# Performance work log

Hardware: AMD Instinct MI355X
Metric: run time of the kernel (lower is better)

The kernel has to match this reference:

```python
import jax, jax.numpy as jnp
import numpy as np
import math

N, D, H, N_BINS, MAX_GRID = 4096, 512, 4, 32, 40

def setup_inputs() -> dict:
    key = jax.random.key(0)
    ks = jax.random.split(key, 12)
    vision_h = jax.random.normal(ks[0], (N, D), dtype=jnp.float32)
    patch_rows = jax.random.randint(ks[1], (N,), 0, MAX_GRID, dtype=jnp.int32)
    patch_cols = jax.random.randint(ks[2], (N,), 0, MAX_GRID, dtype=jnp.int32)
    pos_w = 0.01 * jax.random.normal(ks[3], (D, D), dtype=jnp.float32)
    q_w = 0.02 * jax.random.normal(ks[4], (D, D), dtype=jnp.float32)
    k_w = 0.02 * jax.random.normal(ks[5], (D, D), dtype=jnp.float32)
    v_w = 0.02 * jax.random.normal(ks[6], (D, D), dtype=jnp.float32)
    out_w = 0.02 * jax.random.normal(ks[7], (D, D), dtype=jnp.float32)
    dist_bias = 0.02 * jax.random.normal(ks[8], (H, N_BINS), dtype=jnp.float32)
    gamma_param = jnp.array(0.5, dtype=jnp.float32)
    ln_w = jnp.ones((D,), dtype=jnp.float32)
    ln_b = jnp.zeros((D,), dtype=jnp.float32)
    return {"vision_h": vision_h, "patch_rows": patch_rows, "patch_cols": patch_cols,
            "pos_w": pos_w, "q_w": q_w, "k_w": k_w, "v_w": v_w, "out_w": out_w,
            "dist_bias": dist_bias, "gamma_param": gamma_param, "ln_w": ln_w, "ln_b": ln_b}

def _sin_pe_1d(pos_f, half_dim):
    # pos_f: (N,) float. returns (N, half_dim) with even idx = sin, odd idx = cos
    freq = jnp.exp(jnp.arange(0, half_dim, 2, dtype=jnp.float32) * (-(math.log(10000.0) / half_dim)))
    ang = pos_f[:, None] * freq  # (N, half_dim//2)
    return jnp.stack([jnp.sin(ang), jnp.cos(ang)], axis=-1).reshape(pos_f.shape[0], half_dim)

def reference(vision_h, patch_rows, patch_cols, pos_w, q_w, k_w, v_w, out_w,
              dist_bias, gamma_param, ln_w, ln_b):
    n, d = vision_h.shape
    h = dist_bias.shape[0]
    hd = d // h
    n_bins = dist_bias.shape[1]
    half = d // 2

    rows_f = patch_rows.astype(jnp.float32)
    cols_f = patch_cols.astype(jnp.float32)
    pe = jnp.concatenate([_sin_pe_1d(rows_f, half), _sin_pe_1d(cols_f, half)], axis=-1)  # (N, D)

    h_pos = vision_h + pe @ pos_w.T
    Q = (h_pos @ q_w.T).reshape(n, h, hd).transpose(1, 0, 2)   # (H, N, hd)
    K = (h_pos @ k_w.T).reshape(n, h, hd).transpose(1, 0, 2)
    V = (vision_h @ v_w.T).reshape(n, h, hd).transpose(1, 0, 2)

    logits = jnp.einsum("hnd,hmd->hnm", Q, K) / math.sqrt(hd)   # (H, N, N)

    row_diff = rows_f[:, None] - rows_f[None, :]
    col_diff = cols_f[:, None] - cols_f[None, :]
    dist = jnp.sqrt(row_diff ** 2 + col_diff ** 2)              # (N, N)
    max_log_dist = math.log1p(MAX_GRID * math.sqrt(2.0))
    bins = (jnp.log1p(dist) / max_log_dist * (n_bins - 1)).astype(jnp.int32)
    bins = jnp.clip(bins, 0, n_bins - 1)
    rel_bias = dist_bias[:, bins]                               # (H, N, N)

    attn = jax.nn.softmax(logits + rel_bias, axis=-1)
    attn_out = jnp.einsum("hnm,hmd->hnd", attn, V).transpose(1, 0, 2).reshape(n, d)

    o = attn_out @ out_w.T
    mu = jnp.mean(o, axis=-1, keepdims=True)
    var = jnp.mean((o - mu) ** 2, axis=-1, keepdims=True)
    o_ln = (o - mu) / jnp.sqrt(var + 1e-5) * ln_w + ln_b

    gamma = jax.nn.softplus(gamma_param)
    return vision_h + gamma * o_ln
```

## Files before the change

kernel.cpp:

```cpp
#include <hip/hip_runtime.h>
#include <math.h>

#define N_TOK 4096
#define DMODEL 512
#define NHEAD 4
#define HDIM 128
#define NBINS 32
#define BQ 128
#define BK 64
#define NSPLIT 4
#define KV_PER_SPLIT (N_TOK / NSPLIT)
#define QKSTR 1024

typedef __attribute__((ext_vector_type(8))) short bf16x8;
typedef __attribute__((ext_vector_type(4))) float f32x4;
typedef __attribute__((ext_vector_type(8))) unsigned short u16x8;
typedef __attribute__((ext_vector_type(4))) unsigned short u16x4;

__device__ __forceinline__ unsigned short f2bf(float x) {
    unsigned int u = __float_as_uint(x);
    u += 0x7FFFu + ((u >> 16) & 1u);
    return (unsigned short)(u >> 16);
}
__device__ __forceinline__ float bf2f(unsigned short u) {
    return __uint_as_float(((unsigned int)u) << 16);
}

__global__ __launch_bounds__(256) void pe_prep(const int* __restrict__ rows,
                                               const int* __restrict__ cols,
                                               const float* __restrict__ vh,
                                               unsigned short* __restrict__ pe_bf,
                                               unsigned short* __restrict__ vh_bf) {
    int n = blockIdx.x, t = threadIdx.x;
    float pos = (float)((t < 128) ? rows[n] : cols[n]);
    int k = t & 127;
    float freq = expf(-0.035977892078032f * (float)(2 * k));
    float ang = pos * freq;
    int base = n * DMODEL + ((t < 128) ? 0 : 256) + 2 * k;
    pe_bf[base]     = f2bf(sinf(ang));
    pe_bf[base + 1] = f2bf(cosf(ang));
    float2 v = *(const float2*)&vh[(size_t)n * DMODEL + t * 2];
    vh_bf[(size_t)n * DMODEL + t * 2]     = f2bf(v.x);
    vh_bf[(size_t)n * DMODEL + t * 2 + 1] = f2bf(v.y);
}

__global__ __launch_bounds__(256) void wconv5(const float* __restrict__ w0, const float* __restrict__ w1,
                                              const float* __restrict__ w2, const float* __restrict__ w3,
                                              const float* __restrict__ w4,
                                              unsigned short* __restrict__ dstbase) {
    const float* srcs[5] = {w0, w1, w2, w3, w4};
    const float* src = srcs[blockIdx.y];
    unsigned short* dst = dstbase + (size_t)blockIdx.y * DMODEL * DMODEL;
    int idx = (blockIdx.x * 256 + threadIdx.x) * 4;
    float4 v = *(const float4*)&src[idx];
    u16x4 r;
    r[0] = f2bf(v.x); r[1] = f2bf(v.y); r[2] = f2bf(v.z); r[3] = f2bf(v.w);
    *(u16x4*)&dst[idx] = r;
}

template <bool ADD, bool BF16OUT>
__global__ __launch_bounds__(256) void gemm_mfma(const unsigned short* __restrict__ A,
                                                 const unsigned short* __restrict__ B,
                                                 const float* __restrict__ addv,
                                                 void* __restrict__ Cv,
                                                 int M, int N, int K,
                                                 float scaleA, float scaleB) {
    const int n0 = blockIdx.x * 64;
    const int j0 = blockIdx.y * 128;
    __shared__ unsigned short As[64][72];
    __shared__ unsigned short Bs[128][72];
    const int t    = threadIdx.x;
    const int wid  = t >> 6;
    const int wr   = wid >> 1, wc = wid & 1;
    const int lane = t & 63;
    const int lg   = lane >> 4, li = lane & 15;
    const int str  = t >> 3;
    const int sc   = (t & 7) * 8;

    f32x4 acc[2][4];
#pragma unroll
    for (int i = 0; i < 2; ++i)
#pragma unroll
        for (int j = 0; j < 4; ++j) acc[i][j] = (f32x4){0.f, 0.f, 0.f, 0.f};

    u16x8 areg[2], breg[4];
#pragma unroll
    for (int i = 0; i < 2; ++i)
        areg[i] = *(const u16x8*)&A[(size_t)(n0 + str + i * 32) * K + sc];
#pragma unroll
    for (int i = 0; i < 4; ++i)
        breg[i] = *(const u16x8*)&B[(size_t)(j0 + str + i * 32) * K + sc];

    for (int k0 = 0; k0 < K; k0 += 64) {
        __syncthreads();
#pragma unroll
        for (int i = 0; i < 2; ++i) *(u16x8*)&As[str + i * 32][sc] = areg[i];
#pragma unroll
        for (int i = 0; i < 4; ++i) *(u16x8*)&Bs[str + i * 32][sc] = breg[i];
        __syncthreads();
        if (k0 + 64 < K) {
#pragma unroll
            for (int i = 0; i < 2; ++i)
                areg[i] = *(const u16x8*)&A[(size_t)(n0 + str + i * 32) * K + k0 + 64 + sc];
#pragma unroll
            for (int i = 0; i < 4; ++i)
                breg[i] = *(const u16x8*)&B[(size_t)(j0 + str + i * 32) * K + k0 + 64 + sc];
        }
        __builtin_amdgcn_s_setprio(1);
#pragma unroll
        for (int kc = 0; kc < 2; ++kc) {
            bf16x8 af[2], bfr[4];
#pragma unroll
            for (int mf = 0; mf < 2; ++mf)
                af[mf] = *(const bf16x8*)&As[wr * 32 + mf * 16 + li][kc * 32 + lg * 8];
#pragma unroll
            for (int nf = 0; nf < 4; ++nf)
                bfr[nf] = *(const bf16x8*)&Bs[wc * 64 + nf * 16 + li][kc * 32 + lg * 8];
#pragma unroll
            for (int mf = 0; mf < 2; ++mf)
#pragma unroll
                for (int nf = 0; nf < 4; ++nf)
                    acc[mf][nf] = __builtin_amdgcn_mfma_f32_16x16x32_bf16(af[mf], bfr[nf], acc[mf][nf], 0, 0, 0);
        }
        __builtin_amdgcn_s_setprio(0);
    }
    const float scl = (j0 < 512) ? scaleA : scaleB;
#pragma unroll
    for (int mf = 0; mf < 2; ++mf) {
#pragma unroll
        for (int r = 0; r < 4; ++r) {
            const int row = n0 + wr * 32 + mf * 16 + lg * 4 + r;
#pragma unroll
            for (int nf = 0; nf < 4; ++nf) {
                const int col = j0 + wc * 64 + nf * 16 + li;
                float v = acc[mf][nf][r] * scl;
                if (ADD) v += addv[(size_t)row * N + col];
                if (BF16OUT) ((unsigned short*)Cv)[(size_t)row * N + col] = f2bf(v);
                else         ((float*)Cv)[(size_t)row * N + col] = v;
            }
        }
    }
}

__global__ __launch_bounds__(512, 2) void attn_mfma(const unsigned short* __restrict__ Qb,
                                                    const unsigned short* __restrict__ Kb,
                                                    const unsigned short* __restrict__ Vtb,
                                                    const int* __restrict__ prows,
                                                    const int* __restrict__ pcols,
                                                    const float* __restrict__ dist_bias,
                                                    unsigned short* __restrict__ Opart,
                                                    float* __restrict__ Mp,
                                                    float* __restrict__ Lp) {
    const int h  = blockIdx.y;
    const int n0 = blockIdx.x * BQ;
    const int sp = blockIdx.z;
    __shared__ unsigned short Ks[BK * HDIM];
    __shared__ unsigned short Vts[HDIM * BK];
    __shared__ unsigned short Ps[BQ][68];
    __shared__ unsigned short biasTb[3043];
    __shared__ int krs[BK], kcs[BK];

    const int t    = threadIdx.x;
    const int lane = t & 63;
    const int lg   = lane >> 4;
    const int li   = lane & 15;
    const int qbase = (t >> 6) * 16;

    for (int idx = t; idx < 3043; idx += 512) {
        float d  = sqrtf((float)idx);
        int bin  = (int)(log1pf(d) * (31.0f / 4.0529789877f));
        bin = bin > 31 ? 31 : bin;
        biasTb[idx] = f2bf(dist_bias[h * NBINS + bin]);
    }

    bf16x8 qf[4];
    {
        const unsigned short* qptr = &Qb[(size_t)(n0 + qbase + li) * QKSTR + h * HDIM];
#pragma unroll
        for (int kc = 0; kc < 4; ++kc)
            qf[kc] = *(const bf16x8*)&qptr[kc * 32 + lg * 8];
    }
    const int qrL = prows[n0 + qbase + li];
    const int qcL = pcols[n0 + qbase + li];

    float m_ = -1e30f;
    float l_ = 0.f;
    f32x4 accO[8];
#pragma unroll
    for (int dt = 0; dt < 8; ++dt) accO[dt] = (f32x4){0.f, 0.f, 0.f, 0.f};

    u16x8 kreg[2], vreg[2];
    int krreg = 0, kcreg = 0;
    const int ktr = t >> 4, kch = (t & 15) * 8;
    const int vtr = t >> 3, vch = (t & 7) * 8;

    const int kwofs0 = (ktr * 128 + kch) * 2;
    const int vwofs0 = (vtr * 64 + vch) * 2;

    int m0 = sp * KV_PER_SPLIT;
    {
#pragma unroll
        for (int i = 0; i < 2; ++i)
            kreg[i] = *(const u16x8*)&Kb[(size_t)(m0 + ktr + i * 32) * QKSTR + h * HDIM + kch];
#pragma unroll
        for (int i = 0; i < 2; ++i)
            vreg[i] = *(const u16x8*)&Vtb[(size_t)(h * HDIM + vtr + i * 64) * N_TOK + m0 + vch];
        if (t < BK) { krreg = prows[m0 + t]; kcreg = pcols[m0 + t]; }
    }

    for (int kb = 0; kb < KV_PER_SPLIT / BK; ++kb, m0 += BK) {
        __syncthreads();
#pragma unroll
        for (int i = 0; i < 2; ++i) {
            int ofs = (kwofs0 + i * 32 * 256) ^ ((ktr & 7) << 4);
            *(u16x8*)((char*)Ks + ofs) = kreg[i];
        }
#pragma unroll
        for (int i = 0; i < 2; ++i) {
            int ofs = (vwofs0 + i * 64 * 128) ^ ((vtr & 7) << 4);
            *(u16x8*)((char*)Vts + ofs) = vreg[i];
        }
        if (t < BK) { krs[t] = krreg; kcs[t] = kcreg; }
        __syncthreads();

        if (kb + 1 < KV_PER_SPLIT / BK) {
            const int m1 = m0 + BK;
#pragma unroll
            for (int i = 0; i < 2; ++i)
                kreg[i] = *(const u16x8*)&Kb[(size_t)(m1 + ktr + i * 32) * QKSTR + h * HDIM + kch];
#pragma unroll
            for (int i = 0; i < 2; ++i)
                vreg[i] = *(const u16x8*)&Vtb[(size_t)(h * HDIM + vtr + i * 64) * N_TOK + m1 + vch];
            if (t < BK) { krreg = prows[m1 + t]; kcreg = pcols[m1 + t]; }
        }

        f32x4 s[4];
        __builtin_amdgcn_s_setprio(1);
#pragma unroll
        for (int jt = 0; jt < 4; ++jt) {
            f32x4 acc = {0.f, 0.f, 0.f, 0.f};
#pragma unroll
            for (int kc = 0; kc < 4; ++kc) {
                int ofs = (((jt * 16 + li) * 128 + kc * 32 + lg * 8) * 2) ^ ((li & 7) << 4);
                bf16x8 kf = *(const bf16x8*)((const char*)Ks + ofs);
                acc = __builtin_amdgcn_mfma_f32_16x16x32_bf16(kf, qf[kc], acc, 0, 0, 0);
            }
            s[jt] = acc;
        }
        __builtin_amdgcn_s_setprio(0);

        float p[4][4];
#pragma unroll
        for (int jt = 0; jt < 4; ++jt) {
#pragma unroll
            for (int r = 0; r < 4; ++r) {
                int k  = jt * 16 + lg * 4 + r;
                int dr = qrL - krs[k], dc = qcL - kcs[k];
                p[jt][r] = s[jt][r] + bf2f(biasTb[dr * dr + dc * dc]);
            }
        }

        float t0 = fmaxf(fmaxf(p[0][0], p[0][1]), fmaxf(p[0][2], p[0][3]));
        float t1 = fmaxf(fmaxf(p[1][0], p[1][1]), fmaxf(p[1][2], p[1][3]));
        float t2 = fmaxf(fmaxf(p[2][0], p[2][1]), fmaxf(p[2][2], p[2][3]));
        float t3 = fmaxf(fmaxf(p[3][0], p[3][1]), fmaxf(p[3][2], p[3][3]));
        float pmax = fmaxf(fmaxf(t0, t1), fmaxf(t2, t3));
        pmax = fmaxf(pmax, __shfl_xor(pmax, 16));
        pmax = fmaxf(pmax, __shfl_xor(pmax, 32));

        if (!__all(pmax <= m_ + 8.0f)) {
            float mnew  = fmaxf(m_, pmax);
            float alpha = __expf(m_ - mnew);
            m_ = mnew;
            l_ *= alpha;
            float aq[4];
#pragma unroll
            for (int r = 0; r < 4; ++r)
                aq[r] = __shfl(alpha, (lane & 48) | (lg * 4 + r));
#pragma unroll
            for (int dt = 0; dt < 8; ++dt)
#pragma unroll
                for (int r = 0; r < 4; ++r) accO[dt][r] *= aq[r];
        }

        float rs = 0.f;
#pragma unroll
        for (int jt = 0; jt < 4; ++jt)
#pragma unroll
            for (int r = 0; r < 4; ++r) { p[jt][r] = __expf(p[jt][r] - m_); rs += p[jt][r]; }
        rs += __shfl_xor(rs, 16);
        rs += __shfl_xor(rs, 32);
        l_ += rs;

#pragma unroll
        for (int jt = 0; jt < 4; ++jt) {
            u16x4 w;
#pragma unroll
            for (int r = 0; r < 4; ++r) w[r] = f2bf(p[jt][r]);
            *(u16x4*)&Ps[qbase + li][jt * 16 + lg * 4] = w;
        }

        bf16x8 pf0 = *(const bf16x8*)&Ps[qbase + li][lg * 8];
        bf16x8 pf1 = *(const bf16x8*)&Ps[qbase + li][32 + lg * 8];
        __builtin_amdgcn_s_setprio(1);
#pragma unroll
        for (int dt = 0; dt < 8; ++dt) {
            int ofs0 = (((dt * 16 + li) * 64 + lg * 8) * 2) ^ ((li & 7) << 4);
            bf16x8 vf0 = *(const bf16x8*)((const char*)Vts + ofs0);
            bf16x8 vf1 = *(const bf16x8*)((const char*)Vts + (ofs0 ^ 64));
            accO[dt] = __builtin_amdgcn_mfma_f32_16x16x32_bf16(pf0, vf0, accO[dt], 0, 0, 0);
            accO[dt] = __builtin_amdgcn_mfma_f32_16x16x32_bf16(pf1, vf1, accO[dt], 0, 0, 0);
        }
        __builtin_amdgcn_s_setprio(0);
    }

    float linv[4];
#pragma unroll
    for (int r = 0; r < 4; ++r)
        linv[r] = __shfl(l_, (lane & 48) | (lg * 4 + r));
#pragma unroll
    for (int r = 0; r < 4; ++r) {
        float inv = 1.0f / linv[r];
        int row = n0 + qbase + lg * 4 + r;
#pragma unroll
        for (int dt = 0; dt < 8; ++dt)
            Opart[(size_t)sp * N_TOK * DMODEL + (size_t)row * DMODEL + h * HDIM + dt * 16 + li] =
                f2bf(accO[dt][r] * inv);
    }
    if (lane < 16) {
        int row = n0 + qbase + lane;
        Mp[((size_t)sp * NHEAD + h) * N_TOK + row] = m_;
        Lp[((size_t)sp * NHEAD + h) * N_TOK + row] = l_;
    }
}

__global__ __launch_bounds__(256) void combine_kernel(const unsigned short* __restrict__ Opart,
                                                      const float* __restrict__ Mp,
                                                      const float* __restrict__ Lp,
                                                      unsigned short* __restrict__ outbf) {
    int n = blockIdx.x, t = threadIdx.x;
#pragma unroll
    for (int d0 = t; d0 < DMODEL; d0 += 256) {
        int h = d0 >> 7;
        float mm[NSPLIT], ll[NSPLIT];
        float m = -1e30f;
#pragma unroll
        for (int s = 0; s < NSPLIT; ++s) {
            mm[s] = Mp[((size_t)s * NHEAD + h) * N_TOK + n];
            ll[s] = Lp[((size_t)s * NHEAD + h) * N_TOK + n];
            m = fmaxf(m, mm[s]);
        }
        float acc = 0.f, lsum = 0.f;
#pragma unroll
        for (int s = 0; s < NSPLIT; ++s) {
            float a = __expf(mm[s] - m) * ll[s];
            lsum += a;
            acc += a * bf2f(Opart[(size_t)s * N_TOK * DMODEL + (size_t)n * DMODEL + d0]);
        }
        outbf[(size_t)n * DMODEL + d0] = f2bf(acc / lsum);
    }
}

__global__ __launch_bounds__(256) void final_kernel(const float* __restrict__ o,
                                                    const float* __restrict__ vh,
                                                    const float* __restrict__ lnw,
                                                    const float* __restrict__ lnb,
                                                    const float* __restrict__ gparam,
                                                    float* __restrict__ out) {
    int n = blockIdx.x, t = threadIdx.x;
    size_t base = (size_t)n * DMODEL;
    float x0 = o[base + t], x1 = o[base + t + 256];
    __shared__ float red[4];
    float v = x0 + x1;
#pragma unroll
    for (int off = 32; off > 0; off >>= 1) v += __shfl_down(v, off, 64);
    if ((t & 63) == 0) red[t >> 6] = v;
    __syncthreads();
    float mu = (red[0] + red[1] + red[2] + red[3]) * (1.0f / 512.0f);
    __syncthreads();
    float d0 = x0 - mu, d1 = x1 - mu;
    v = d0 * d0 + d1 * d1;
#pragma unroll
    for (int off = 32; off > 0; off >>= 1) v += __shfl_down(v, off, 64);
    if ((t & 63) == 0) red[t >> 6] = v;
    __syncthreads();
    float var  = (red[0] + red[1] + red[2] + red[3]) * (1.0f / 512.0f);
    float rstd = rsqrtf(var + 1e-5f);
    float gamma = log1pf(expf(gparam[0]));
    out[base + t]       = vh[base + t]       + gamma * (d0 * rstd * lnw[t]       + lnb[t]);
    out[base + t + 256] = vh[base + t + 256] + gamma * (d1 * rstd * lnw[t + 256] + lnb[t + 256]);
}

extern "C" void kernel_launch(void* const* d_in, const int* in_sizes, int n_in,
                              void* d_out, int out_size, void* d_ws, size_t ws_size,
                              hipStream_t stream) {
    const float* vision_h  = (const float*)d_in[0];
    const int*   prows     = (const int*)d_in[1];
    const int*   pcols     = (const int*)d_in[2];
    const float* pos_w     = (const float*)d_in[3];
    const float* q_w       = (const float*)d_in[4];
    const float* k_w       = (const float*)d_in[5];
    const float* v_w       = (const float*)d_in[6];
    const float* out_w     = (const float*)d_in[7];
    const float* dist_bias = (const float*)d_in[8];
    const float* gamma_p   = (const float*)d_in[9];
    const float* ln_w      = (const float*)d_in[10];
    const float* ln_b      = (const float*)d_in[11];
    float* out = (float*)d_out;
    char* base = (char*)d_ws;

    const size_t MB = 1024 * 1024;
    unsigned short* pe_bf   = (unsigned short*)(base + 0);
    unsigned short* vh_bf   = (unsigned short*)(base + 4  * MB);
    unsigned short* hpos_bf = (unsigned short*)(base + 8  * MB);
    unsigned short* Opart   = (unsigned short*)(base + 0);
    float*          ob      = (float*)(base + 0);
    unsigned short* QKb     = (unsigned short*)(base + 16 * MB);
    unsigned short* Vtb     = (unsigned short*)(base + 24 * MB);
    unsigned short* attn_bf = (unsigned short*)(base + 28 * MB);
    float*          Mp      = (float*)(base + 32 * MB);
    float*          Lp      = (float*)(base + 32 * MB + 262144);
    unsigned short* wbf     = (unsigned short*)(base + 32 * MB + 524288);

    unsigned short* w_pos = wbf;
    unsigned short* w_q   = wbf + 1 * DMODEL * DMODEL;
    unsigned short* w_v   = wbf + 3 * DMODEL * DMODEL;
    unsigned short* w_o   = wbf + 4 * DMODEL * DMODEL;

    const float qscale = 0.08838834764831845f;

    pe_prep<<<N_TOK, 256, 0, stream>>>(prows, pcols, vision_h, pe_bf, vh_bf);
    wconv5<<<dim3(256, 5), 256, 0, stream>>>(pos_w, q_w, k_w, v_w, out_w, wbf);
    gemm_mfma<true,  true ><<<dim3(64, 4), 256, 0, stream>>>(pe_bf, w_pos, vision_h, hpos_bf,
                                                             N_TOK, DMODEL, DMODEL, 1.0f, 1.0f);
    gemm_mfma<false, true ><<<dim3(64, 8), 256, 0, stream>>>(hpos_bf, w_q, nullptr, QKb,
                                                             N_TOK, 1024, DMODEL, qscale, 1.0f);
    gemm_mfma<false, true ><<<dim3(8, 32), 256, 0, stream>>>(w_v, vh_bf, nullptr, Vtb,
                                                             DMODEL, N_TOK, DMODEL, 1.0f, 1.0f);
    attn_mfma<<<dim3(N_TOK / BQ, NHEAD, NSPLIT), 512, 0, stream>>>(QKb, QKb + 512, Vtb, prows, pcols,
                                                                   dist_bias, Opart, Mp, Lp);
    combine_kernel<<<N_TOK, 256, 0, stream>>>(Opart, Mp, Lp, attn_bf);
    gemm_mfma<false, false><<<dim3(64, 4), 256, 0, stream>>>(attn_bf, w_o, nullptr, ob,
                                                             N_TOK, DMODEL, DMODEL, 1.0f, 1.0f);
    final_kernel<<<N_TOK, 256, 0, stream>>>(ob, vision_h, ln_w, ln_b, gamma_p, out);
}
```

Before: 146.8 us.

## Precompute positional-projection table per grid coordinate instead of per-token GEMM

Positions take only 40 distinct row and 40 distinct column values, so pe @ pos_w.T is computed once per coordinate into an 80x512 fp32 table. A gather kernel then forms h_pos = vision_h + row_contrib + col_contrib in bf16. This replaces the per-token PE generation and the N×D×D GEMM, and drops the pe_bf buffer. It also swaps the software bf16 rounding of attention probabilities for a hardware conversion. The table is computed in fp32, so numerics shift slightly compared with the bf16 GEMM path.

```diff
diff --git a/kernel.cpp b/kernel.cpp
--- a/kernel.cpp
+++ b/kernel.cpp
@@ -11,6 +11,7 @@
 #define NSPLIT 4
 #define KV_PER_SPLIT (N_TOK / NSPLIT)
 #define QKSTR 1024
+#define MAXG 40
 
 typedef __attribute__((ext_vector_type(8))) short bf16x8;
 typedef __attribute__((ext_vector_type(4))) float f32x4;
@@ -22,26 +23,14 @@
     u += 0x7FFFu + ((u >> 16) & 1u);
     return (unsigned short)(u >> 16);
 }
+__device__ __forceinline__ unsigned short f2bf_hw(float x) {
+    __bf16 b = (__bf16)x;
+    union { __bf16 h; unsigned short u; } c;
+    c.h = b;
+    return c.u;
+}
 __device__ __forceinline__ float bf2f(unsigned short u) {
     return __uint_as_float(((unsigned int)u) << 16);
-}
-
-__global__ __launch_bounds__(256) void pe_prep(const int* __restrict__ rows,
-                                               const int* __restrict__ cols,
-                                               const float* __restrict__ vh,
-                                               unsigned short* __restrict__ pe_bf,
-                                               unsigned short* __restrict__ vh_bf) {
-    int n = blockIdx.x, t = threadIdx.x;
-    float pos = (float)((t < 128) ? rows[n] : cols[n]);
-    int k = t & 127;
-    float freq = expf(-0.035977892078032f * (float)(2 * k));
-    float ang = pos * freq;
-    int base = n * DMODEL + ((t < 128) ? 0 : 256) + 2 * k;
-    pe_bf[base]     = f2bf(sinf(ang));
-    pe_bf[base + 1] = f2bf(cosf(ang));
-    float2 v = *(const float2*)&vh[(size_t)n * DMODEL + t * 2];
-    vh_bf[(size_t)n * DMODEL + t * 2]     = f2bf(v.x);
-    vh_bf[(size_t)n * DMODEL + t * 2 + 1] = f2bf(v.y);
 }
 
 __global__ __launch_bounds__(256) void wconv5(const float* __restrict__ w0, const float* __restrict__ w1,
@@ -56,6 +45,54 @@
     u16x4 r;
     r[0] = f2bf(v.x); r[1] = f2bf(v.y); r[2] = f2bf(v.z); r[3] = f2bf(v.w);
     *(u16x4*)&dst[idx] = r;
+}
+
+__global__ __launch_bounds__(256) void pos_contrib(const float* __restrict__ pos_w,
+                                                   float* __restrict__ contrib) {
+    const int p = blockIdx.x;
+    const int t = threadIdx.x;
+    const bool isRow = p < MAXG;
+    const float pos = (float)(isRow ? p : p - MAXG);
+    __shared__ float pe[256];
+    {
+        int k = t >> 1;
+        float freq = expf(-0.035977892078032f * (float)(2 * k));
+        float ang = pos * freq;
+        pe[t] = (t & 1) ? cosf(ang) : sinf(ang);
+    }
+    __syncthreads();
+    const int jofs = isRow ? 0 : 256;
+#pragma unroll
+    for (int cc = 0; cc < 2; ++cc) {
+        int c = t + cc * 256;
+        const float* wrow = &pos_w[(size_t)c * DMODEL + jofs];
+        float acc = 0.f;
+        for (int j = 0; j < 256; j += 4) {
+            float4 w4 = *(const float4*)&wrow[j];
+            acc += pe[j] * w4.x + pe[j + 1] * w4.y + pe[j + 2] * w4.z + pe[j + 3] * w4.w;
+        }
+        contrib[(size_t)p * DMODEL + c] = acc;
+    }
+}
+
+__global__ __launch_bounds__(256) void hpos_kernel(const int* __restrict__ rows,
+                                                   const int* __restrict__ cols,
+                                                   const float* __restrict__ vh,
+                                                   const float* __restrict__ contrib,
+                                                   unsigned short* __restrict__ vh_bf,
+                                                   unsigned short* __restrict__ hpos_bf) {
+    const int n = blockIdx.x, t = threadIdx.x;
+    const float* rc = &contrib[(size_t)rows[n] * DMODEL];
+    const float* cc = &contrib[(size_t)(MAXG + cols[n]) * DMODEL];
+    const size_t base = (size_t)n * DMODEL;
+    const int c = t * 2;
+    float2 v = *(const float2*)&vh[base + c];
+    vh_bf[base + c]     = f2bf(v.x);
+    vh_bf[base + c + 1] = f2bf(v.y);
+    float2 r = *(const float2*)&rc[c];
+    float2 cl = *(const float2*)&cc[c];
+    hpos_bf[base + c]     = f2bf(v.x + r.x + cl.x);
+    hpos_bf[base + c + 1] = f2bf(v.y + r.y + cl.y);
 }
 
 template <bool ADD, bool BF16OUT>
@@ -296,7 +333,7 @@
         for (int jt = 0; jt < 4; ++jt) {
             u16x4 w;
 #pragma unroll
-            for (int r = 0; r < 4; ++r) w[r] = f2bf(p[jt][r]);
+            for (int r = 0; r < 4; ++r) w[r] = f2bf_hw(p[jt][r]);
             *(u16x4*)&Ps[qbase + li][jt * 16 + lg * 4] = w;
         }
 
@@ -410,7 +447,6 @@
     char* base = (char*)d_ws;
 
     const size_t MB = 1024 * 1024;
-    unsigned short* pe_bf   = (unsigned short*)(base + 0);
     unsigned short* vh_bf   = (unsigned short*)(base + 4  * MB);
     unsigned short* hpos_bf = (unsigned short*)(base + 8  * MB);
     unsigned short* Opart   = (unsigned short*)(base + 0);
@@ -421,18 +457,19 @@
     float*          Mp      = (float*)(base + 32 * MB);
     float*          Lp      = (float*)(base + 32 * MB + 262144);
     unsigned short* wbf     = (unsigned short*)(base + 32 * MB + 524288);
+    float*          contrib = (float*)(base + 35 * MB);
 
     unsigned short* w_pos = wbf;
     unsigned short* w_q   = wbf + 1 * DMODEL * DMODEL;
     unsigned short* w_v   = wbf + 3 * DMODEL * DMODEL;
     unsigned short* w_o   = wbf + 4 * DMODEL * DMODEL;
+    (void)w_pos;
 
     const float qscale = 0.08838834764831845f;
 
-    pe_prep<<<N_TOK, 256, 0, stream>>>(prows, pcols, vision_h, pe_bf, vh_bf);
     wconv5<<<dim3(256, 5), 256, 0, stream>>>(pos_w, q_w, k_w, v_w, out_w, wbf);
-    gemm_mfma<true,  true ><<<dim3(64, 4), 256, 0, stream>>>(pe_bf, w_pos, vision_h, hpos_bf,
-                                                             N_TOK, DMODEL, DMODEL, 1.0f, 1.0f);
+    pos_contrib<<<2 * MAXG, 256, 0, stream>>>(pos_w, contrib);
+    hpos_kernel<<<N_TOK, 256, 0, stream>>>(prows, pcols, vision_h, contrib, vh_bf, hpos_bf);
     gemm_mfma<false, true ><<<dim3(64, 8), 256, 0, stream>>>(hpos_bf, w_q, nullptr, QKb,
                                                              N_TOK, 1024, DMODEL, qscale, 1.0f);
     gemm_mfma<false, true ><<<dim3(8, 32), 256, 0, stream>>>(w_v, vh_bf, nullptr, Vtb,
```

After: 155.8 us. 6.1% more time.
